# Performance work log

Hardware: AMD Instinct MI355X
Metric: run time of the kernel (lower is better)

Reference implementation:

```python
import jax, jax.numpy as jnp
import numpy as np

N_NODES = 51200      # 128 graphs * 400 ROIs
N_ROI = 400
HID = 64             # 'batch_size' arg of the torch module = hidden channels = n_timepoints
N_EDGES = 1638400    # avg degree 32
N_CLASSES = 2
NEG_SLOPE = 0.01


def setup_inputs():
    key = jax.random.key(0)
    ks = jax.random.split(key, 20)
    s = 0.05
    inp = {
        'x': jax.random.normal(ks[0], (N_NODES, HID), dtype=jnp.float32),
        'edge_index': jax.random.randint(ks[1], (2, N_EDGES), 0, N_NODES, dtype=jnp.int64),
        'edge_weight': jax.random.uniform(ks[2], (N_EDGES,), dtype=jnp.float32),
        # GCNConv weights stored [in, out]; biases [out]
        'W1': jax.random.normal(ks[3], (HID, HID), dtype=jnp.float32) * s,
        'b1': jnp.zeros((HID,), jnp.float32),
        'W2': jax.random.normal(ks[4], (HID, HID), dtype=jnp.float32) * s,
        'b2': jnp.zeros((HID,), jnp.float32),
        'W3': jax.random.normal(ks[5], (HID, HID), dtype=jnp.float32) * s,
        'b3': jnp.zeros((HID,), jnp.float32),
        'W4': jax.random.normal(ks[6], (HID, HID), dtype=jnp.float32) * s,
        'b4': jnp.zeros((HID,), jnp.float32),
        'fc1_w': jax.random.normal(ks[7], (N_ROI * HID, 256), dtype=jnp.float32) * 0.01,
        'fc1_b': jnp.zeros((256,), jnp.float32),
        'fc2_w': jax.random.normal(ks[8], (256, 128), dtype=jnp.float32) * s,
        'fc2_b': jnp.zeros((128,), jnp.float32),
        'fc3_w': jax.random.normal(ks[9], (128, N_CLASSES), dtype=jnp.float32) * s,
        'fc3_b': jnp.zeros((N_CLASSES,), jnp.float32),
    }
    return inp


def _gcn_norm(edge_index, edge_weight, n):
    # PyG GCNConv: add self-loops (weight 1), symmetric D^-1/2 A D^-1/2 normalization
    loop = jnp.arange(n, dtype=edge_index.dtype)
    src = jnp.concatenate([edge_index[0], loop])
    dst = jnp.concatenate([edge_index[1], loop])
    w = jnp.concatenate([edge_weight, jnp.ones((n,), edge_weight.dtype)])
    deg = jax.ops.segment_sum(w, dst, num_segments=n)
    dis = jnp.where(deg > 0, jax.lax.rsqrt(jnp.maximum(deg, 1e-30)), 0.0)
    norm = dis[src] * w * dis[dst]
    return src, dst, norm


def _conv(h, W, b, src, dst, norm, n):
    h = h @ W                                   # [N, out]
    msg = h[src] * norm[:, None]                # gather + scale
    out = jax.ops.segment_sum(msg, dst, num_segments=n) + b
    return out


def _leaky(v):
    return jnp.where(v >= 0, v, NEG_SLOPE * v)


def _head(h, fc1_w, fc1_b, fc2_w, fc2_b, fc3_w, fc3_b):
    # global_mean_pool with batch = arange(N) is identity; pool == reshape to graphs
    g = h.reshape(-1, N_ROI * HID)              # [G, n_roi*hid]
    g = g @ fc1_w + fc1_b                       # dropout is eval-mode identity
    g = g @ fc2_w + fc2_b
    g = g @ fc3_w + fc3_b
    return g


def reference(x, edge_index, edge_weight, W1, b1, W2, b2, W3, b3, W4, b4,
              fc1_w, fc1_b, fc2_w, fc2_b, fc3_w, fc3_b):
    n = x.shape[0]
    src, dst, norm = _gcn_norm(edge_index, edge_weight, n)
    h = _leaky(_conv(x, W1, b1, src, dst, norm, n))
    h = _leaky(_conv(h, W2, b2, src, dst, norm, n))
    h = _leaky(_conv(h, W3, b3, src, dst, norm, n))
    h = _leaky(_conv(h, W4, b4, src, dst, norm, n))
    logits = _head(h, fc1_w, fc1_b, fc2_w, fc2_b, fc3_w, fc3_b)
    logits0 = _head(x, fc1_w, fc1_b, fc2_w, fc2_b, fc3_w, fc3_b)
    penal = 0.09 * logits.shape[0] / jnp.linalg.norm(logits - logits0)
    return logits, penal
```

## Files before the change

### kernel.cpp

```cpp
#include <hip/hip_runtime.h>
#include <cstddef>

#define N_NODES 51200
#define N_EDGES 1638400
#define HID 64
#define N_ROI 400
#define N_GRAPHS 128
#define KHEAD 25600
#define NEG_SLOPE 0.01f
#define CAP 80
#define NCHUNK 200
#define CHUNK 8192
#define NBIN 1024
#define BINSZ 50
#define LSTRIDE 81

typedef unsigned short u16;
typedef unsigned int u32;
typedef unsigned char u8;
typedef float f32x2 __attribute__((ext_vector_type(2)));

__device__ inline u16 f2bf(float f) {
    u32 u = __float_as_uint(f);
    u32 r = u + 0x7FFFu + ((u >> 16) & 1u);
    return (u16)(r >> 16);
}
__device__ inline float bf2f(u16 h) { return __uint_as_float(((u32)h) << 16); }

__device__ inline f32x2 dec8lo(u32 v) { return __builtin_amdgcn_cvt_pk_f32_fp8((int)v, false); }
__device__ inline f32x2 dec8hi(u32 v) { return __builtin_amdgcn_cvt_pk_f32_fp8((int)v, true); }
template <bool HI>
__device__ inline u32 enc8(float a, float b, u32 old) {
    return (u32)__builtin_amdgcn_cvt_pk_fp8_f32(a, b, (int)old, HI);
}
__device__ inline u32 pack4_fp8(float a, float b, float c, float d) {
    u32 w = enc8<false>(a, b, 0u);
    return enc8<true>(c, d, w);
}


__global__ __launch_bounds__(1024) void k1(const int* __restrict__ ei,
                                           const float* __restrict__ ew,
                                           uint2* __restrict__ chunkData,
                                           u32* __restrict__ offcnt,
                                           const float* __restrict__ x,
                                           u8* __restrict__ x8,
                                           const float* __restrict__ fc2w,
                                           const float* __restrict__ fc3w,
                                           const float* __restrict__ fc1b,
                                           const float* __restrict__ fc2b,
                                           const float* __restrict__ fc3b,
                                           float* __restrict__ fc23,
                                           float* __restrict__ bc) {
    int bid = blockIdx.x, t = threadIdx.x;
    __shared__ u32 cnt[NBIN];
    __shared__ u32 cur[NBIN];
    __shared__ u32 wsum[16];
    __shared__ uint2 stag[CHUNK];
    __shared__ float t1[128];

    if (bid < NCHUNK) {
        cnt[t] = 0;
        __syncthreads();
        int base = bid * CHUNK;
        const int4* sp = reinterpret_cast<const int4*>(ei + base);
        const int4* dp = reinterpret_cast<const int4*>(ei + N_EDGES + base);
        const float4* wp = reinterpret_cast<const float4*>(ew + base);
        int4 sa = sp[2 * t], sb = sp[2 * t + 1];
        int4 da = dp[2 * t], db = dp[2 * t + 1];
        float4 wa = wp[2 * t], wb = wp[2 * t + 1];
        int ss[8] = {sa.x, sa.y, sa.z, sa.w, sb.x, sb.y, sb.z, sb.w};
        int dd[8] = {da.x, da.y, da.z, da.w, db.x, db.y, db.z, db.w};
        float wv[8] = {wa.x, wa.y, wa.z, wa.w, wb.x, wb.y, wb.z, wb.w};
        u32 lo[8]; int bin[8];
        #pragma unroll
        for (int i = 0; i < 8; i++) {
            int b = (int)((u32)dd[i] / BINSZ);
            bin[i] = b;
            lo[i] = (u32)ss[i] | ((u32)(dd[i] - b * BINSZ) << 16);
            atomicAdd(&cnt[b], 1u);
        }
        __syncthreads();
        int wave = t >> 6, lane = t & 63;
        u32 v = cnt[t], inc = v;
        #pragma unroll
        for (int d = 1; d < 64; d <<= 1) {
            u32 o = __shfl_up(inc, d, 64);
            if (lane >= d) inc += o;
        }
        if (lane == 63) wsum[wave] = inc;
        __syncthreads();
        if (t == 0) {
            u32 r = 0;
            #pragma unroll
            for (int i = 0; i < 16; i++) { u32 c = wsum[i]; wsum[i] = r; r += c; }
        }
        __syncthreads();
        u32 excl = inc - v + wsum[wave];
        cur[t] = excl;
        offcnt[(size_t)bid * NBIN + t] = excl | (v << 16);
        __syncthreads();
        #pragma unroll
        for (int i = 0; i < 8; i++) {
            u32 pos = atomicAdd(&cur[bin[i]], 1u);
            stag[pos] = make_uint2(lo[i], __float_as_uint(wv[i]));
        }
        __syncthreads();
        const uint4* sg4 = reinterpret_cast<const uint4*>(stag);
        uint4* out4 = reinterpret_cast<uint4*>(chunkData + (size_t)base);
        #pragma unroll
        for (int i = 0; i < 4; i++) out4[i * 1024 + t] = sg4[i * 1024 + t];
    } else if (bid < 400) {
        int idx = (bid - NCHUNK) * 1024 + t;
        const float4* xp = reinterpret_cast<const float4*>(x) + (size_t)idx * 4;
        float4 a = xp[0], b = xp[1], c = xp[2], d = xp[3];
        reinterpret_cast<uint4*>(x8)[idx] =
            make_uint4(pack4_fp8(a.x, a.y, a.z, a.w), pack4_fp8(b.x, b.y, b.z, b.w),
                       pack4_fp8(c.x, c.y, c.z, c.w), pack4_fp8(d.x, d.y, d.z, d.w));
    } else {
        if (t < 256) {
            float s0 = 0.f, s1 = 0.f;
            const float* row = fc2w + t * 128;
            for (int j = 0; j < 128; j++) {
                float a = row[j];
                s0 += a * fc3w[2 * j];
                s1 += a * fc3w[2 * j + 1];
            }
            fc23[2 * t] = s0;
            fc23[2 * t + 1] = s1;
        }
        if (t < 128) {
            float s = fc2b[t];
            for (int k = 0; k < 256; k++) s += fc1b[k] * fc2w[k * 128 + t];
            t1[t] = s;
        }
        __syncthreads();
        if (t < 2) {
            float s = fc3b[t];
            for (int j = 0; j < 128; j++) s += t1[j] * fc3w[2 * j + t];
            bc[t] = s;
        }
    }
}


__global__ __launch_bounds__(256) void k1t(const u32* __restrict__ in,
                                           u32* __restrict__ outT) {
    __shared__ u32 tile[32][33];
    int bx = blockIdx.x & 31, cy = blockIdx.x >> 5;
    int b0 = bx * 32, c0 = cy * 32;
    int tx = threadIdx.x & 31, ty = threadIdx.x >> 5;
    for (int i = ty; i < 32; i += 8) {
        int c = c0 + i;
        if (c < NCHUNK) tile[i][tx] = in[(size_t)c * NBIN + b0 + tx];
    }
    __syncthreads();
    for (int i = ty; i < 32; i += 8) {
        int b = b0 + i;
        int c = c0 + tx;
        if (c < NCHUNK) outT[(size_t)b * NCHUNK + c] = tile[tx][i];
    }
}


__global__ __launch_bounds__(512) void k2(const uint2* __restrict__ chunkData,
                                          const u32* __restrict__ offcntT,
                                          u32* __restrict__ buck,
                                          int* __restrict__ cnts,
                                          float* __restrict__ dis,
                                          const float* __restrict__ fc1w,
                                          const float* __restrict__ fc23,
                                          float* __restrict__ Wc) {
    int bid = blockIdx.x, t = threadIdx.x;
    __shared__ u32 lbuck[BINSZ * LSTRIDE];
    __shared__ u32 lcnt[BINSZ];
    __shared__ float ldeg[BINSZ];
    __shared__ u32 oc[NCHUNK];

    if (bid < NBIN) {
        if (t < BINSZ) { lcnt[t] = 0; ldeg[t] = 0.f; }
        if (t < NCHUNK) oc[t] = offcntT[(size_t)bid * NCHUNK + t];
        __syncthreads();
        int w = t >> 6, lane = t & 63;
        int sBase = w * 25;
        for (int j = 0; j < 32; j += 8) {
            int so = j + (lane >> 3);
            int s = sBase + so;
            int i0 = lane & 7;
            int k = 0, off = 0;
            if (so < 25) {
                u32 o = oc[s];
                off = (int)(o & 0xffffu);
                k = (int)(o >> 16);
            }
            const uint2* cd = chunkData + (size_t)s * CHUNK + off;
            for (int i = i0; i < k; i += 8) {
                uint2 e = cd[i];
                u32 node = e.x >> 16;
                u32 src = e.x & 0xffffu;
                float ww = __uint_as_float(e.y);
                u32 pos = atomicAdd(&lcnt[node], 1u);
                if (pos < CAP - 1) lbuck[node * LSTRIDE + pos] = ((u32)f2bf(ww) << 16) | src;
                atomicAdd(&ldeg[node], ww);
            }
        }
        __syncthreads();
        int sg = t >> 5, ln = t & 31;
        for (int n = sg; n < BINSZ; n += 16) {
            int node = bid * BINSZ + n;
            int k = min((int)lcnt[n], CAP - 1);
            u32* dst = buck + (size_t)node * CAP;
            for (int i = ln; i < k; i += 32) dst[i] = lbuck[n * LSTRIDE + i];
            if (ln == 0) {
                cnts[node] = k;
                dis[node] = rsqrtf(1.f + ldeg[n]);
            }
        }
    } else {
        float* f23 = (float*)lbuck;
        f23[t] = fc23[t];
        __syncthreads();
        int r = (bid - NBIN) * 512 + t;
        const float* row = fc1w + (size_t)r * 256;
        float s0 = 0.f, s1 = 0.f;
        #pragma unroll 8
        for (int k = 0; k < 256; k++) {
            float a = row[k];
            s0 += a * f23[2 * k];
            s1 += a * f23[2 * k + 1];
        }
        Wc[2 * r] = s0;
        Wc[2 * r + 1] = s1;
    }
}


__global__ __launch_bounds__(1024) void k3(u32* __restrict__ buck,
                                           int* __restrict__ cnts,
                                           const float* __restrict__ dis) {
    int gt = blockIdx.x * 1024 + threadIdx.x;
    int node = gt >> 5, sub = gt & 31;
    float d = dis[node];
    int k = cnts[node];
    u32* bk = buck + (size_t)node * CAP;
    for (int j = sub; j < k; j += 32) {
        u32 e = bk[j];
        float val = bf2f((u16)(e >> 16)) * d * dis[e & 0xffffu];
        bk[j] = ((u32)f2bf(val) << 16) | (e & 0xffffu);
    }
    if (sub == 0) {
        bk[k] = ((u32)f2bf(d * d) << 16) | (u32)node;
        cnts[node] = k + 1;
    }
}


__global__ __launch_bounds__(512) void k_layer(const u8* __restrict__ H8,
                                               const u32* __restrict__ buck,
                                               const int* __restrict__ cnts,
                                               const float* __restrict__ W,
                                               const float* __restrict__ bias,
                                               u8* __restrict__ Hout) {
    __shared__ float Ws[64][64];
    __shared__ float ZsT[64][33];
    int t = threadIdx.x;
    int base = blockIdx.x * 32;

    #pragma unroll
    for (int i = 0; i < 2; i++) {
        int f = t + i * 512;
        int kk = f >> 4, c4 = f & 15;
        float4 wv = reinterpret_cast<const float4*>(W)[f];
        *reinterpret_cast<float4*>(&Ws[kk][c4 * 4]) = wv;
    }

    int grp = t >> 4, sub = t & 15;
    int node = base + grp;
    int k = cnts[node];
    const u32* bk = buck + (size_t)node * CAP;
    const u32* H32 = reinterpret_cast<const u32*>(H8);
    float a0 = 0.f, a1 = 0.f, a2 = 0.f, a3 = 0.f;
    for (int j0 = 0; j0 < k; j0 += 16) {
        int idx = j0 + sub;
        u32 pre = (idx < k) ? bk[idx] : 0u;
        #pragma unroll
        for (int i = 0; i < 16; i++) {
            u32 e = (u32)__shfl((int)pre, i, 16);
            float val = __uint_as_float(e & 0xffff0000u);
            u32 src = e & 0xffffu;
            u32 r = H32[src * 16 + sub];
            f32x2 lo = dec8lo(r), hi = dec8hi(r);
            a0 += val * lo.x; a1 += val * lo.y;
            a2 += val * hi.x; a3 += val * hi.y;
        }
    }
    ZsT[4 * sub + 0][grp] = a0;
    ZsT[4 * sub + 1][grp] = a1;
    ZsT[4 * sub + 2][grp] = a2;
    ZsT[4 * sub + 3][grp] = a3;
    __syncthreads();

    int r = t >> 4, c4 = t & 15;
    float4 acc = {0.f, 0.f, 0.f, 0.f};
    #pragma unroll 8
    for (int kk = 0; kk < 64; kk++) {
        float a = ZsT[kk][r];
        const float4 w = *reinterpret_cast<const float4*>(&Ws[kk][c4 * 4]);
        acc.x += a * w.x; acc.y += a * w.y; acc.z += a * w.z; acc.w += a * w.w;
    }
    float4 bb = reinterpret_cast<const float4*>(bias)[c4];
    float v0 = acc.x + bb.x, v1 = acc.y + bb.y, v2 = acc.z + bb.z, v3 = acc.w + bb.w;
    v0 = v0 >= 0.f ? v0 : NEG_SLOPE * v0;
    v1 = v1 >= 0.f ? v1 : NEG_SLOPE * v1;
    v2 = v2 >= 0.f ? v2 : NEG_SLOPE * v2;
    v3 = v3 >= 0.f ? v3 : NEG_SLOPE * v3;
    *reinterpret_cast<u32*>(Hout + (size_t)(base + r) * HID + c4 * 4) =
        pack4_fp8(v0, v1, v2, v3);
}


__global__ __launch_bounds__(256) void k_logits(const u8* __restrict__ h4,
                                                const float* __restrict__ x,
                                                const float* __restrict__ Wc,
                                                const float* __restrict__ bc,
                                                float* __restrict__ out,
                                                float* __restrict__ sq,
                                                int* __restrict__ done) {
    int g = blockIdx.x, t = threadIdx.x;
    const u8* bh = h4 + (size_t)g * KHEAD;
    const float* bx = x + (size_t)g * KHEAD;
    float aH0 = 0.f, aH1 = 0.f, aX0 = 0.f, aX1 = 0.f;
    for (int k2 = t; k2 < KHEAD / 2; k2 += 256) {
        u32 hv = reinterpret_cast<const u16*>(bh)[k2];
        f32x2 h = dec8lo(hv);
        float2 xv = reinterpret_cast<const float2*>(bx)[k2];
        float4 wc = reinterpret_cast<const float4*>(Wc)[k2];
        aH0 += h.x * wc.x + h.y * wc.z;
        aH1 += h.x * wc.y + h.y * wc.w;
        aX0 += xv.x * wc.x + xv.y * wc.z;
        aX1 += xv.x * wc.y + xv.y * wc.w;
    }
    for (int off = 32; off > 0; off >>= 1) {
        aH0 += __shfl_down(aH0, off);
        aH1 += __shfl_down(aH1, off);
        aX0 += __shfl_down(aX0, off);
        aX1 += __shfl_down(aX1, off);
    }
    __shared__ float red[4][4];
    int wave = t >> 6, lane = t & 63;
    if (lane == 0) {
        red[wave][0] = aH0; red[wave][1] = aH1;
        red[wave][2] = aX0; red[wave][3] = aX1;
    }
    __syncthreads();
    if (t == 0) {
        float h0 = red[0][0] + red[1][0] + red[2][0] + red[3][0];
        float h1 = red[0][1] + red[1][1] + red[2][1] + red[3][1];
        float x0 = red[0][2] + red[1][2] + red[2][2] + red[3][2];
        float x1 = red[0][3] + red[1][3] + red[2][3] + red[3][3];
        out[2 * g]     = h0 + bc[0];
        out[2 * g + 1] = h1 + bc[1];
        float d0 = h0 - x0, d1 = h1 - x1;
        atomicAdd(sq, d0 * d0 + d1 * d1);
        __threadfence();
        int c = atomicAdd(done, 1);
        if (c == N_GRAPHS - 1) {
            __threadfence();
            float s = atomicAdd(sq, 0.f);
            out[2 * N_GRAPHS] = 0.09f * (float)N_GRAPHS / sqrtf(s);
        }
    }
}


extern "C" void kernel_launch(void* const* d_in, const int* in_sizes, int n_in,
                              void* d_out, int out_size, void* d_ws, size_t ws_size,
                              hipStream_t stream) {
    const float* x    = (const float*)d_in[0];
    const int*   ei   = (const int*)d_in[1];
    const float* ew   = (const float*)d_in[2];
    const float* W1   = (const float*)d_in[3];
    const float* b1   = (const float*)d_in[4];
    const float* W2   = (const float*)d_in[5];
    const float* b2   = (const float*)d_in[6];
    const float* W3   = (const float*)d_in[7];
    const float* b3   = (const float*)d_in[8];
    const float* W4   = (const float*)d_in[9];
    const float* b4   = (const float*)d_in[10];
    const float* fc1w = (const float*)d_in[11];
    const float* fc1b = (const float*)d_in[12];
    const float* fc2w = (const float*)d_in[13];
    const float* fc2b = (const float*)d_in[14];
    const float* fc3w = (const float*)d_in[15];
    const float* fc3b = (const float*)d_in[16];
    float* out = (float*)d_out;

    char* base = (char*)d_ws;
    size_t off = 0;
    auto alloc = [&](size_t bytes) -> void* {
        void* p = base + off;
        off += (bytes + 255) & ~(size_t)255;
        return p;
    };
    uint2* chunkData = (uint2*)alloc((size_t)N_EDGES * 8);
    u32*   offcnt    = (u32*)alloc((size_t)NCHUNK * NBIN * 4);
    u32*   offcntT   = (u32*)alloc((size_t)NCHUNK * NBIN * 4);
    u32*   buck      = (u32*)alloc((size_t)N_NODES * CAP * 4);
    int*   cnts      = (int*)alloc((size_t)N_NODES * 4);
    float* dis       = (float*)alloc((size_t)N_NODES * 4);
    u8*    x8        = (u8*)alloc((size_t)N_NODES * HID);
    u8*    ha        = (u8*)alloc((size_t)N_NODES * HID);
    u8*    hb        = (u8*)alloc((size_t)N_NODES * HID);
    float* fc23      = (float*)alloc(512 * 4);
    float* bc        = (float*)alloc(2 * 4);
    float* Wc        = (float*)alloc((size_t)KHEAD * 2 * 4);
    char*  ctrl      = (char*)alloc(256);
    float* sq        = (float*)ctrl;
    int*   done      = (int*)(ctrl + 4);

    (void)hipMemsetAsync(ctrl, 0, 8, stream);
    k1<<<401, 1024, 0, stream>>>(ei, ew, chunkData, offcnt, x, x8,
                                 fc2w, fc3w, fc1b, fc2b, fc3b, fc23, bc);
    k1t<<<224, 256, 0, stream>>>(offcnt, offcntT);
    k2<<<NBIN + 50, 512, 0, stream>>>(chunkData, offcntT, buck, cnts, dis,
                                      fc1w, fc23, Wc);
    k3<<<1600, 1024, 0, stream>>>(buck, cnts, dis);

    const float* Wl[4] = {W1, W2, W3, W4};
    const float* bl[4] = {b1, b2, b3, b4};
    u8* hbufs[2] = {ha, hb};
    const u8* hin = x8;
    for (int l = 0; l < 4; l++) {
        u8* hout = hbufs[l & 1];
        k_layer<<<N_NODES / 32, 512, 0, stream>>>(hin, buck, cnts,
                                                  Wl[l], bl[l], hout);
        hin = hout;
    }

    k_logits<<<N_GRAPHS, 256, 0, stream>>>(hin, x, Wc, bc, out, sq, done);
}
```

Baseline: 192.8 us.

## Widen per-lane gathers in GCN layer and split fc1 fold across lanes

The layer kernel now assigns 8 lanes per node, each gathering 8 bytes of the FP8 feature row with a uint2 load, so a block covers 64 nodes with twice the accumulators per thread. The dense 64x64 transform is widened to 8 outputs per thread to match. Separately, the fc1·fc23 fold in k2 is spread across 400 blocks, with 8 lanes per row using float4 loads and a shuffle reduction instead of one thread per full 256-wide row. The aim is fewer, wider memory transactions and better coalescing, at the cost of more registers per thread and fewer blocks in the layer kernel.

Result: faster. 183.8 us (-4.7%).

```diff
diff --git a/kernel.cpp b/kernel.cpp
--- a/kernel.cpp
+++ b/kernel.cpp
@@ -14,6 +14,7 @@
 #define NBIN 1024
 #define BINSZ 50
 #define LSTRIDE 81
+#define NWC 400
 
 typedef unsigned short u16;
 typedef unsigned int u32;
@@ -220,17 +221,25 @@
         float* f23 = (float*)lbuck;
         f23[t] = fc23[t];
         __syncthreads();
-        int r = (bid - NBIN) * 512 + t;
-        const float* row = fc1w + (size_t)r * 256;
+        const float2* f2p = reinterpret_cast<const float2*>(f23);
+        int row = (bid - NBIN) * 64 + (t >> 3);
+        int p = t & 7;
+        const float4* rp = reinterpret_cast<const float4*>(fc1w + (size_t)row * 256 + p * 32);
         float s0 = 0.f, s1 = 0.f;
-        #pragma unroll 8
-        for (int k = 0; k < 256; k++) {
-            float a = row[k];
-            s0 += a * f23[2 * k];
-            s1 += a * f23[2 * k + 1];
-        }
-        Wc[2 * r] = s0;
-        Wc[2 * r + 1] = s1;
+        #pragma unroll
+        for (int i = 0; i < 8; i++) {
+            float4 a = rp[i];
+            int kb = p * 32 + i * 4;
+            float2 w0 = f2p[kb], w1 = f2p[kb + 1], w2 = f2p[kb + 2], w3 = f2p[kb + 3];
+            s0 += a.x * w0.x + a.y * w1.x + a.z * w2.x + a.w * w3.x;
+            s1 += a.x * w0.y + a.y * w1.y + a.z * w2.y + a.w * w3.y;
+        }
+        #pragma unroll
+        for (int off = 4; off; off >>= 1) {
+            s0 += __shfl_down(s0, off, 8);
+            s1 += __shfl_down(s1, off, 8);
+        }
+        if (p == 0) reinterpret_cast<float2*>(Wc)[row] = make_float2(s0, s1);
     }
 }
 
@@ -262,9 +271,9 @@
                                                const float* __restrict__ bias,
                                                u8* __restrict__ Hout) {
     __shared__ float Ws[64][64];
-    __shared__ float ZsT[64][33];
+    __shared__ float ZsT[64][65];
     int t = threadIdx.x;
-    int base = blockIdx.x * 32;
+    int base = blockIdx.x * 64;
 
     #pragma unroll
     for (int i = 0; i < 2; i++) {
@@ -274,48 +283,58 @@
         *reinterpret_cast<float4*>(&Ws[kk][c4 * 4]) = wv;
     }
 
-    int grp = t >> 4, sub = t & 15;
+    int grp = t >> 3, sub = t & 7;
     int node = base + grp;
     int k = cnts[node];
     const u32* bk = buck + (size_t)node * CAP;
-    const u32* H32 = reinterpret_cast<const u32*>(H8);
+    const uint2* H64 = reinterpret_cast<const uint2*>(H8);
     float a0 = 0.f, a1 = 0.f, a2 = 0.f, a3 = 0.f;
-    for (int j0 = 0; j0 < k; j0 += 16) {
+    float a4 = 0.f, a5 = 0.f, a6 = 0.f, a7 = 0.f;
+    for (int j0 = 0; j0 < k; j0 += 8) {
         int idx = j0 + sub;
         u32 pre = (idx < k) ? bk[idx] : 0u;
         #pragma unroll
-        for (int i = 0; i < 16; i++) {
-            u32 e = (u32)__shfl((int)pre, i, 16);
+        for (int i = 0; i < 8; i++) {
+            u32 e = (u32)__shfl((int)pre, i, 8);
             float val = __uint_as_float(e & 0xffff0000u);
             u32 src = e & 0xffffu;
-            u32 r = H32[src * 16 + sub];
-            f32x2 lo = dec8lo(r), hi = dec8hi(r);
-            a0 += val * lo.x; a1 += val * lo.y;
-            a2 += val * hi.x; a3 += val * hi.y;
-        }
-    }
-    ZsT[4 * sub + 0][grp] = a0;
-    ZsT[4 * sub + 1][grp] = a1;
-    ZsT[4 * sub + 2][grp] = a2;
-    ZsT[4 * sub + 3][grp] = a3;
+            uint2 r = H64[(size_t)src * 8 + sub];
+            f32x2 l0 = dec8lo(r.x), h0 = dec8hi(r.x);
+            f32x2 l1 = dec8lo(r.y), h1 = dec8hi(r.y);
+            a0 += val * l0.x; a1 += val * l0.y; a2 += val * h0.x; a3 += val * h0.y;
+            a4 += val * l1.x; a5 += val * l1.y; a6 += val * h1.x; a7 += val * h1.y;
+        }
+    }
+    ZsT[8 * sub + 0][grp] = a0; ZsT[8 * sub + 1][grp] = a1;
+    ZsT[8 * sub + 2][grp] = a2; ZsT[8 * sub + 3][grp] = a3;
+    ZsT[8 * sub + 4][grp] = a4; ZsT[8 * sub + 5][grp] = a5;
+    ZsT[8 * sub + 6][grp] = a6; ZsT[8 * sub + 7][grp] = a7;
     __syncthreads();
 
-    int r = t >> 4, c4 = t & 15;
-    float4 acc = {0.f, 0.f, 0.f, 0.f};
+    int r = t >> 3, c0 = (t & 7) * 8;
+    float4 acc0 = {0,0,0,0}, acc1 = {0,0,0,0};
     #pragma unroll 8
     for (int kk = 0; kk < 64; kk++) {
-        float a = ZsT[kk][r];
-        const float4 w = *reinterpret_cast<const float4*>(&Ws[kk][c4 * 4]);
-        acc.x += a * w.x; acc.y += a * w.y; acc.z += a * w.z; acc.w += a * w.w;
-    }
-    float4 bb = reinterpret_cast<const float4*>(bias)[c4];
-    float v0 = acc.x + bb.x, v1 = acc.y + bb.y, v2 = acc.z + bb.z, v3 = acc.w + bb.w;
+        float z = ZsT[kk][r];
+        float4 w0 = *reinterpret_cast<const float4*>(&Ws[kk][c0]);
+        float4 w1 = *reinterpret_cast<const float4*>(&Ws[kk][c0 + 4]);
+        acc0.x += z * w0.x; acc0.y += z * w0.y; acc0.z += z * w0.z; acc0.w += z * w0.w;
+        acc1.x += z * w1.x; acc1.y += z * w1.y; acc1.z += z * w1.z; acc1.w += z * w1.w;
+    }
+    float4 b0 = reinterpret_cast<const float4*>(bias)[(c0 >> 2)];
+    float4 b1 = reinterpret_cast<const float4*>(bias)[(c0 >> 2) + 1];
+    float v0 = acc0.x + b0.x, v1 = acc0.y + b0.y, v2 = acc0.z + b0.z, v3 = acc0.w + b0.w;
+    float v4 = acc1.x + b1.x, v5 = acc1.y + b1.y, v6 = acc1.z + b1.z, v7 = acc1.w + b1.w;
     v0 = v0 >= 0.f ? v0 : NEG_SLOPE * v0;
     v1 = v1 >= 0.f ? v1 : NEG_SLOPE * v1;
     v2 = v2 >= 0.f ? v2 : NEG_SLOPE * v2;
     v3 = v3 >= 0.f ? v3 : NEG_SLOPE * v3;
-    *reinterpret_cast<u32*>(Hout + (size_t)(base + r) * HID + c4 * 4) =
-        pack4_fp8(v0, v1, v2, v3);
+    v4 = v4 >= 0.f ? v4 : NEG_SLOPE * v4;
+    v5 = v5 >= 0.f ? v5 : NEG_SLOPE * v5;
+    v6 = v6 >= 0.f ? v6 : NEG_SLOPE * v6;
+    v7 = v7 >= 0.f ? v7 : NEG_SLOPE * v7;
+    *reinterpret_cast<uint2*>(Hout + (size_t)(base + r) * HID + c0) =
+        make_uint2(pack4_fp8(v0, v1, v2, v3), pack4_fp8(v4, v5, v6, v7));
 }
 
 
@@ -422,8 +441,8 @@
     k1<<<401, 1024, 0, stream>>>(ei, ew, chunkData, offcnt, x, x8,
                                  fc2w, fc3w, fc1b, fc2b, fc3b, fc23, bc);
     k1t<<<224, 256, 0, stream>>>(offcnt, offcntT);
-    k2<<<NBIN + 50, 512, 0, stream>>>(chunkData, offcntT, buck, cnts, dis,
-                                      fc1w, fc23, Wc);
+    k2<<<NBIN + NWC, 512, 0, stream>>>(chunkData, offcntT, buck, cnts, dis,
+                                       fc1w, fc23, Wc);
     k3<<<1600, 1024, 0, stream>>>(buck, cnts, dis);
 
     const float* Wl[4] = {W1, W2, W3, W4};
@@ -432,7 +451,7 @@
     const u8* hin = x8;
     for (int l = 0; l < 4; l++) {
         u8* hout = hbufs[l & 1];
-        k_layer<<<N_NODES / 32, 512, 0, stream>>>(hin, buck, cnts,
+        k_layer<<<N_NODES / 64, 512, 0, stream>>>(hin, buck, cnts,
                                                   Wl[l], bl[l], hout);
         hin = hout;
     }
```
